# Performance work log

Measured on AMD Instinct MI355X. Metric: run time of the kernel, lower is better.

Reference implementation:

```python
import jax, jax.numpy as jnp
import numpy as np

NUM_ITERS = 20  # fixed in the original forward: transcribe(dna, iterations=20)


def transcribe(dna_seed, dna_a, dna_b):
    """Fractal DNA decompression: 20 elementwise contractive-map iterations
    over the full weight tensor, starting from the DNA seed."""
    def step(w, ab):
        a, b = ab
        w = a * w + b * jnp.sin(w)
        return w, None
    w, _ = jax.lax.scan(step, dna_seed, (dna_a, dna_b))
    return w  # [out_features, in_features]


def setup_inputs() -> dict:
    key = jax.random.key(0)
    k1, k2, k3, k4, k5 = jax.random.split(key, 5)
    TOKENS, IN_F, OUT_F = 2048, 4096, 4096
    return {
        "x": jax.random.normal(k1, (TOKENS, IN_F), dtype=jnp.float32),
        "dna_seed": jax.random.normal(k2, (OUT_F, IN_F), dtype=jnp.float32),
        "dna_a": jax.random.uniform(k3, (NUM_ITERS,), dtype=jnp.float32),
        "dna_b": jax.random.uniform(k4, (NUM_ITERS,), dtype=jnp.float32),
        "bias": jax.random.normal(k5, (OUT_F,), dtype=jnp.float32),
    }


def reference(x, dna_seed, dna_a, dna_b, bias):
    weight = transcribe(dna_seed, dna_a, dna_b)          # [out, in]
    # F.linear(x, weight, bias) == x @ weight.T + bias
    return jnp.einsum('ti,oi->to', x, weight) + bias     # [tokens, out]
```

## Files before the change

### kernel.cpp

```cpp
#include <hip/hip_runtime.h>

typedef __attribute__((ext_vector_type(8))) short short8;
typedef __attribute__((ext_vector_type(4))) float floatx4;
typedef __attribute__((ext_vector_type(2))) float float2v;

#define TOKENS 2048
#define IN_F   4096
#define OUT_F  4096
#define NITER  20

#define INV_2PI 0.15915494309189535f
#define TWO_PI  6.283185307179586f

__device__ __forceinline__ unsigned short f2bf(float f) {
    unsigned int u = __builtin_bit_cast(unsigned int, f);
    u += 0x7fffu + ((u >> 16) & 1u);
    return (unsigned short)(u >> 16);
}

__device__ __forceinline__ void step2(float2v& v, float2v a2, float2v bc2) {
    float2v s;
    s.x = __builtin_amdgcn_sinf(v.x);
    s.y = __builtin_amdgcn_sinf(v.y);
    v = __builtin_elementwise_fma(bc2, s, v * a2);
}

#define WBLOCKS (OUT_F * IN_F / 8 / 256)
#define XBLOCKS (TOKENS * IN_F / 8 / 256)

__global__ __launch_bounds__(256) void transcribe_fused_kernel(
    const float4* __restrict__ seed, const float4* __restrict__ xin,
    const float* __restrict__ da, const float* __restrict__ db,
    short8* __restrict__ w_out, short8* __restrict__ x_out)
{
    const int b = blockIdx.x;
    short8 o;
    if (b < WBLOCKS) {
        int i = b * 256 + threadIdx.x;
        float4 U = seed[2 * i];
        float4 V = seed[2 * i + 1];
        float2v p0 = {U.x, U.y}, p1 = {U.z, U.w};
        float2v p2 = {V.x, V.y}, p3 = {V.z, V.w};
        const float2v kinv = {INV_2PI, INV_2PI};
        p0 *= kinv; p1 *= kinv; p2 *= kinv; p3 *= kinv;
#pragma unroll
        for (int t = 0; t < NITER; t++) {
            float a = da[t], bc = db[t] * INV_2PI;
            float2v a2 = {a, a}, bc2 = {bc, bc};
            step2(p0, a2, bc2);
            step2(p1, a2, bc2);
            step2(p2, a2, bc2);
            step2(p3, a2, bc2);
        }
        o[0] = (short)f2bf(p0.x * TWO_PI); o[1] = (short)f2bf(p0.y * TWO_PI);
        o[2] = (short)f2bf(p1.x * TWO_PI); o[3] = (short)f2bf(p1.y * TWO_PI);
        o[4] = (short)f2bf(p2.x * TWO_PI); o[5] = (short)f2bf(p2.y * TWO_PI);
        o[6] = (short)f2bf(p3.x * TWO_PI); o[7] = (short)f2bf(p3.y * TWO_PI);
        w_out[i] = o;
    } else {
        int i = (b - WBLOCKS) * 256 + threadIdx.x;
        float4 u = xin[2 * i];
        float4 v = xin[2 * i + 1];
        o[0] = (short)f2bf(u.x); o[1] = (short)f2bf(u.y);
        o[2] = (short)f2bf(u.z); o[3] = (short)f2bf(u.w);
        o[4] = (short)f2bf(v.x); o[5] = (short)f2bf(v.y);
        o[6] = (short)f2bf(v.z); o[7] = (short)f2bf(v.w);
        x_out[i] = o;
    }
}

__device__ __forceinline__ void g2l16(const ushort* g, ushort* l) {
    __builtin_amdgcn_global_load_lds(
        (const __attribute__((address_space(1))) unsigned int*)g,
        (__attribute__((address_space(3))) unsigned int*)l, 16, 0, 0);
}

#define BK     64
#define BM     256
#define BN     128
#define NT     (IN_F / BK)
#define ASLOT  (BM * BK)
#define BSLOT  (BN * BK)
#define LDS_BYTES (3 * (ASLOT + BSLOT) * 2)

__global__ __launch_bounds__(512, 2) void gemm_bt_kernel(
    const ushort* __restrict__ A,
    const ushort* __restrict__ B,
    const float* __restrict__ bias,
    float* __restrict__ C)
{
    extern __shared__ ushort lds[];
    ushort* As = lds;
    ushort* Bs = lds + 3 * ASLOT;

    const int tid  = threadIdx.x;
    const int lane = tid & 63;
    const int wid  = tid >> 6;
    const int g    = wid >> 2;
    const int w2   = wid & 3;
    const int wm   = (w2 >> 1) << 7;
    const int wn   = (w2 & 1) << 6;
    const int fm   = lane & 15;
    const int q    = lane >> 4;

    const int bid = blockIdx.x;
    const int jj  = bid >> 3;
    const int bn  = (bid & 7) * 4 + (jj & 3);
    const int bm  = jj >> 2;

    const int gcol = (((lane & 7) ^ (lane >> 3)) << 3);

    const ushort* gA = A + (size_t)(bm * BM) * IN_F;
    const ushort* gB = B + (size_t)(bn * BN) * IN_F;

    floatx4 acc[8][4];
#pragma unroll
    for (int i = 0; i < 8; i++)
#pragma unroll
        for (int j = 0; j < 4; j++)
            acc[i][j] = (floatx4){0.f, 0.f, 0.f, 0.f};

#define STAGE(k0v, sl)                                                        \
    {                                                                         \
        _Pragma("unroll")                                                     \
        for (int u = 0; u < 4; u++) {                                         \
            const int cb = ((u << 3) | wid) << 6;                             \
            const int r  = (cb >> 3) + (lane >> 3);                           \
            g2l16(gA + (size_t)r * IN_F + (k0v) + gcol,                       \
                  As + (sl) * ASLOT + cb * 8 + lane * 8);                     \
        }                                                                     \
        _Pragma("unroll")                                                     \
        for (int u = 0; u < 2; u++) {                                         \
            const int cb = ((u << 3) | wid) << 6;                             \
            const int r  = (cb >> 3) + (lane >> 3);                           \
            g2l16(gB + (size_t)r * IN_F + (k0v) + gcol,                       \
                  Bs + (sl) * BSLOT + cb * 8 + lane * 8);                     \
        }                                                                     \
    }

#define LOADFRAG(sl)                                                          \
    const int sa = (((q + 4 * g) & 7) ^ (fm & 7)) << 3;                       \
    _Pragma("unroll")                                                         \
    for (int i = 0; i < 8; i++)                                               \
        af[i] = *(const short8*)(As + (sl) * ASLOT + (wm + i * 16 + fm) * BK + sa); \
    _Pragma("unroll")                                                         \
    for (int j = 0; j < 4; j++)                                               \
        bf[j] = *(const short8*)(Bs + (sl) * BSLOT + (wn + j * 16 + fm) * BK + sa);

#define MFMA32()                                                              \
    __builtin_amdgcn_s_setprio(1);                                            \
    _Pragma("unroll")                                                         \
    for (int i = 0; i < 8; i++)                                               \
        _Pragma("unroll")                                                     \
        for (int j = 0; j < 4; j++)                                           \
            acc[i][j] = __builtin_amdgcn_mfma_f32_16x16x32_bf16(              \
                af[i], bf[j], acc[i][j], 0, 0, 0);                            \
    __builtin_amdgcn_s_setprio(0);

#define TILE_MAIN(vm, sl, k3)                                                 \
    {                                                                         \
        asm volatile("s_waitcnt vmcnt(" #vm ")" ::: "memory");                \
        __builtin_amdgcn_s_barrier();                                         \
        short8 af[8], bf[4];                                                  \
        LOADFRAG(sl);                                                         \
        asm volatile("s_waitcnt lgkmcnt(0)" ::: "memory");                    \
        __builtin_amdgcn_s_barrier();                                         \
        STAGE(k3, sl);                                                        \
        __builtin_amdgcn_sched_barrier(0);                                    \
        MFMA32();                                                             \
    }

#define TILE_TAIL(vm, sl)                                                     \
    {                                                                         \
        asm volatile("s_waitcnt vmcnt(" #vm ")" ::: "memory");                \
        __builtin_amdgcn_s_barrier();                                         \
        short8 af[8], bf[4];                                                  \
        LOADFRAG(sl);                                                         \
        MFMA32();                                                             \
    }

    STAGE(0 * BK, 0);
    STAGE(1 * BK, 1);
    STAGE(2 * BK, 2);

    int st   = 0;
    int kpre = 3 * BK;
#pragma unroll 1
    for (int t = 0; t <= NT - 4; ++t) {
        TILE_MAIN(12, st, kpre);
        kpre += BK;
        st = (st == 2) ? 0 : st + 1;
    }
    TILE_TAIL(12, 1);
    TILE_TAIL(6, 2);
    TILE_TAIL(0, 0);

#undef STAGE
#undef LOADFRAG
#undef MFMA32
#undef TILE_MAIN
#undef TILE_TAIL

    __syncthreads();
    floatx4* red = (floatx4*)lds;
    if (g == 1) {
#pragma unroll
        for (int i = 0; i < 8; i++)
#pragma unroll
            for (int j = 0; j < 4; j++)
                red[(size_t)(w2 * 32 + i * 4 + j) * 64 + lane] = acc[i][j];
    }
    __syncthreads();
    if (g == 0) {
        const int cn = lane & 15;
        const int cm = (lane >> 4) << 2;
        float bv[4];
#pragma unroll
        for (int j = 0; j < 4; j++)
            bv[j] = bias[bn * BN + wn + j * 16 + cn];
#pragma unroll
        for (int i = 0; i < 8; i++) {
#pragma unroll
            for (int j = 0; j < 4; j++) {
                floatx4 p = red[(size_t)(w2 * 32 + i * 4 + j) * 64 + lane];
#pragma unroll
                for (int r = 0; r < 4; r++) acc[i][j][r] += p[r];
            }
#pragma unroll
            for (int r = 0; r < 4; r++) {
                int m = bm * BM + wm + i * 16 + cm + r;
                float* crow = C + (size_t)m * OUT_F + bn * BN + wn + cn;
#pragma unroll
                for (int j = 0; j < 4; j++)
                    crow[j * 16] = acc[i][j][r] + bv[j];
            }
        }
    }
}

extern "C" void kernel_launch(void* const* d_in, const int* in_sizes, int n_in,
                              void* d_out, int out_size, void* d_ws, size_t ws_size,
                              hipStream_t stream) {
    const float* x    = (const float*)d_in[0];
    const float* seed = (const float*)d_in[1];
    const float* da   = (const float*)d_in[2];
    const float* db   = (const float*)d_in[3];
    const float* bias = (const float*)d_in[4];
    float* out        = (float*)d_out;

    ushort* w_bf = (ushort*)d_ws;
    ushort* x_bf = w_bf + (size_t)OUT_F * IN_F;

    static bool lds_attr_set = false;
    if (!lds_attr_set) {
        hipFuncSetAttribute(reinterpret_cast<const void*>(gemm_bt_kernel),
                            hipFuncAttributeMaxDynamicSharedMemorySize,
                            LDS_BYTES);
        lds_attr_set = true;
    }

    transcribe_fused_kernel<<<WBLOCKS + XBLOCKS, 256, 0, stream>>>(
        (const float4*)seed, (const float4*)x, da, db,
        (short8*)w_bf, (short8*)x_bf);

    gemm_bt_kernel<<<dim3(32 * 8), dim3(512), LDS_BYTES, stream>>>(
        x_bf, w_bf, bias, out);
}
```

Baseline: 208.0 us.

## Split K in half and overlap second-half transcription with first-half GEMM

The transcription kernel now only produces the first half of the K dimension. A new mid kernel runs the first-half GEMM with 8 waves while 4 extra producer waves per block transcribe the second half of W and convert the second half of X to bf16. A final kernel accumulates the second-half GEMM into the output. This hides the sin-heavy transcription of half the weights behind MFMA work, but adds a read-modify-write of the output, one more launch, and a larger block (768 threads) that may reduce occupancy.

```diff
diff --git a/kernel.cpp b/kernel.cpp
--- a/kernel.cpp
+++ b/kernel.cpp
@@ -25,48 +25,86 @@
     v = __builtin_elementwise_fma(bc2, s, v * a2);
 }
 
-#define WBLOCKS (OUT_F * IN_F / 8 / 256)
-#define XBLOCKS (TOKENS * IN_F / 8 / 256)
-
-__global__ __launch_bounds__(256) void transcribe_fused_kernel(
-    const float4* __restrict__ seed, const float4* __restrict__ xin,
+
+#define T1_WBLK 4096
+#define T1_XBLK 2048
+
+__global__ __launch_bounds__(256) void transcribe_h1_kernel(
+    const float* __restrict__ seed, const float* __restrict__ xin,
     const float* __restrict__ da, const float* __restrict__ db,
-    short8* __restrict__ w_out, short8* __restrict__ x_out)
+    ushort* __restrict__ w_bf, ushort* __restrict__ x_bf)
 {
     const int b = blockIdx.x;
     short8 o;
-    if (b < WBLOCKS) {
-        int i = b * 256 + threadIdx.x;
-        float4 U = seed[2 * i];
-        float4 V = seed[2 * i + 1];
-        float2v p0 = {U.x, U.y}, p1 = {U.z, U.w};
-        float2v p2 = {V.x, V.y}, p3 = {V.z, V.w};
-        const float2v kinv = {INV_2PI, INV_2PI};
-        p0 *= kinv; p1 *= kinv; p2 *= kinv; p3 *= kinv;
+    if (b < T1_WBLK) {
+        const int i   = b * 256 + threadIdx.x;
+        const int row = i >> 8;
+        const int col = (i & 255) << 3;
+        const float* src = seed + (size_t)row * IN_F + col;
+        const float4 U = *(const float4*)src;
+        const float4 V = *(const float4*)(src + 4);
+        float2v p0 = {U.x * INV_2PI, U.y * INV_2PI};
+        float2v p1 = {U.z * INV_2PI, U.w * INV_2PI};
+        float2v p2 = {V.x * INV_2PI, V.y * INV_2PI};
+        float2v p3 = {V.z * INV_2PI, V.w * INV_2PI};
 #pragma unroll
         for (int t = 0; t < NITER; t++) {
-            float a = da[t], bc = db[t] * INV_2PI;
-            float2v a2 = {a, a}, bc2 = {bc, bc};
-            step2(p0, a2, bc2);
-            step2(p1, a2, bc2);
-            step2(p2, a2, bc2);
-            step2(p3, a2, bc2);
+            const float a = da[t], bc = db[t] * INV_2PI;
+            const float2v a2 = {a, a}, bc2 = {bc, bc};
+            step2(p0, a2, bc2); step2(p1, a2, bc2);
+            step2(p2, a2, bc2); step2(p3, a2, bc2);
         }
         o[0] = (short)f2bf(p0.x * TWO_PI); o[1] = (short)f2bf(p0.y * TWO_PI);
         o[2] = (short)f2bf(p1.x * TWO_PI); o[3] = (short)f2bf(p1.y * TWO_PI);
         o[4] = (short)f2bf(p2.x * TWO_PI); o[5] = (short)f2bf(p2.y * TWO_PI);
         o[6] = (short)f2bf(p3.x * TWO_PI); o[7] = (short)f2bf(p3.y * TWO_PI);
-        w_out[i] = o;
+        *(short8*)(w_bf + (size_t)row * IN_F + col) = o;
     } else {
-        int i = (b - WBLOCKS) * 256 + threadIdx.x;
-        float4 u = xin[2 * i];
-        float4 v = xin[2 * i + 1];
+        const int i   = (b - T1_WBLK) * 256 + threadIdx.x;
+        const int row = i >> 8;
+        const int col = (i & 255) << 3;
+        const float* src = xin + (size_t)row * IN_F + col;
+        const float4 u = *(const float4*)src;
+        const float4 v = *(const float4*)(src + 4);
         o[0] = (short)f2bf(u.x); o[1] = (short)f2bf(u.y);
         o[2] = (short)f2bf(u.z); o[3] = (short)f2bf(u.w);
         o[4] = (short)f2bf(v.x); o[5] = (short)f2bf(v.y);
         o[6] = (short)f2bf(v.z); o[7] = (short)f2bf(v.w);
-        x_out[i] = o;
-    }
+        *(short8*)(x_bf + (size_t)row * IN_F + col) = o;
+    }
+}
+
+__device__ __forceinline__ void produceW_f4(
+    int idx, const float* __restrict__ seed,
+    const float* __restrict__ da, const float* __restrict__ db,
+    ushort* __restrict__ w_bf)
+{
+    const int row = idx >> 9;
+    const int col = 2048 + ((idx & 511) << 2);
+    const float4 v = *(const float4*)(seed + (size_t)row * IN_F + col);
+    float2v p0 = {v.x * INV_2PI, v.y * INV_2PI};
+    float2v p1 = {v.z * INV_2PI, v.w * INV_2PI};
+#pragma unroll
+    for (int t = 0; t < NITER; t++) {
+        const float a = da[t], bc = db[t] * INV_2PI;
+        const float2v a2 = {a, a}, bc2 = {bc, bc};
+        step2(p0, a2, bc2); step2(p1, a2, bc2);
+    }
+    ushort4 o;
+    o.x = f2bf(p0.x * TWO_PI); o.y = f2bf(p0.y * TWO_PI);
+    o.z = f2bf(p1.x * TWO_PI); o.w = f2bf(p1.y * TWO_PI);
+    *(ushort4*)(w_bf + (size_t)row * IN_F + col) = o;
+}
+
+__device__ __forceinline__ void produceX_f4(
+    int idx, const float* __restrict__ xin, ushort* __restrict__ x_bf)
+{
+    const int row = idx >> 9;
+    const int col = 2048 + ((idx & 511) << 2);
+    const float4 v = *(const float4*)(xin + (size_t)row * IN_F + col);
+    ushort4 o;
+    o.x = f2bf(v.x); o.y = f2bf(v.y); o.z = f2bf(v.z); o.w = f2bf(v.w);
+    *(ushort4*)(x_bf + (size_t)row * IN_F + col) = o;
 }
 
 __device__ __forceinline__ void g2l16(const ushort* g, ushort* l) {
@@ -78,15 +116,182 @@
 #define BK     64
 #define BM     256
 #define BN     128
-#define NT     (IN_F / BK)
+#define NT2    32
 #define ASLOT  (BM * BK)
 #define BSLOT  (BN * BK)
 #define LDS_BYTES (3 * (ASLOT + BSLOT) * 2)
 
-__global__ __launch_bounds__(512, 2) void gemm_bt_kernel(
+#define STAGE(k0v, sl)                                                        \
+    {                                                                         \
+        _Pragma("unroll")                                                     \
+        for (int u = 0; u < 4; u++) {                                         \
+            const int cb = ((u << 3) | wid) << 6;                             \
+            const int r  = (cb >> 3) + (lane >> 3);                           \
+            g2l16(gA + (size_t)r * IN_F + (k0v) + gcol,                       \
+                  As + (sl) * ASLOT + cb * 8 + lane * 8);                     \
+        }                                                                     \
+        _Pragma("unroll")                                                     \
+        for (int u = 0; u < 2; u++) {                                         \
+            const int cb = ((u << 3) | wid) << 6;                             \
+            const int r  = (cb >> 3) + (lane >> 3);                           \
+            g2l16(gB + (size_t)r * IN_F + (k0v) + gcol,                       \
+                  Bs + (sl) * BSLOT + cb * 8 + lane * 8);                     \
+        }                                                                     \
+    }
+
+#define LOADFRAG(sl)                                                          \
+    const int sa = (((q + 4 * g) & 7) ^ (fm & 7)) << 3;                       \
+    _Pragma("unroll")                                                         \
+    for (int i = 0; i < 8; i++)                                               \
+        af[i] = *(const short8*)(As + (sl) * ASLOT + (wm + i * 16 + fm) * BK + sa); \
+    _Pragma("unroll")                                                         \
+    for (int j = 0; j < 4; j++)                                               \
+        bf[j] = *(const short8*)(Bs + (sl) * BSLOT + (wn + j * 16 + fm) * BK + sa);
+
+#define MFMA32()                                                              \
+    __builtin_amdgcn_s_setprio(1);                                            \
+    _Pragma("unroll")                                                         \
+    for (int i = 0; i < 8; i++)                                               \
+        _Pragma("unroll")                                                     \
+        for (int j = 0; j < 4; j++)                                           \
+            acc[i][j] = __builtin_amdgcn_mfma_f32_16x16x32_bf16(              \
+                af[i], bf[j], acc[i][j], 0, 0, 0);                            \
+    __builtin_amdgcn_s_setprio(0);
+
+#define GEMM_BODY()                                                           \
+    floatx4 acc[8][4];                                                        \
+    _Pragma("unroll")                                                         \
+    for (int i = 0; i < 8; i++)                                               \
+        _Pragma("unroll")                                                     \
+        for (int j = 0; j < 4; j++)                                           \
+            acc[i][j] = (floatx4){0.f, 0.f, 0.f, 0.f};                        \
+    STAGE(0 * BK, 0);                                                         \
+    STAGE(1 * BK, 1);                                                         \
+    STAGE(2 * BK, 2);                                                         \
+    int st   = 0;                                                             \
+    int kpre = 3 * BK;                                                        \
+    _Pragma("unroll 1")                                                       \
+    for (int t = 0; t <= NT2 - 4; ++t) {    \
+        asm volatile("s_waitcnt vmcnt(12)" ::: "memory");                     \
+        __builtin_amdgcn_s_barrier();                                         \
+        short8 af[8], bf[4];                                                  \
+        LOADFRAG(st);                                                         \
+        asm volatile("s_waitcnt lgkmcnt(0)" ::: "memory");                    \
+        __builtin_amdgcn_s_barrier();                                         \
+        STAGE(kpre, st);                                                      \
+        __builtin_amdgcn_sched_barrier(0);                                    \
+        MFMA32();                                                             \
+        kpre += BK;                                                           \
+        st = (st == 2) ? 0 : st + 1;                                          \
+    }                                                                         \
+                \
+    {                                                                         \
+        asm volatile("s_waitcnt vmcnt(12)" ::: "memory");                     \
+        __builtin_amdgcn_s_barrier();                                         \
+        short8 af[8], bf[4];                                                  \
+        LOADFRAG(2);                                                          \
+        MFMA32();                                                             \
+    }                                                                         \
+    {                                                                         \
+        asm volatile("s_waitcnt vmcnt(6)" ::: "memory");                      \
+        __builtin_amdgcn_s_barrier();                                         \
+        short8 af[8], bf[4];                                                  \
+        LOADFRAG(0);                                                          \
+        MFMA32();                                                             \
+    }                                                                         \
+    {                                                                         \
+        asm volatile("s_waitcnt vmcnt(0)" ::: "memory");                      \
+        __builtin_amdgcn_s_barrier();                                         \
+        short8 af[8], bf[4];                                                  \
+        LOADFRAG(1);                                                          \
+        MFMA32();                                                             \
+    }                                                                         \
+               \
+    __syncthreads();                                                          \
+    floatx4* red = (floatx4*)lds;                                             \
+    if (g == 1) {                                                             \
+        _Pragma("unroll")                                                     \
+        for (int i = 0; i < 8; i++)                                           \
+            _Pragma("unroll")                                                 \
+            for (int j = 0; j < 4; j++)                                       \
+                red[(size_t)(w2 * 32 + i * 4 + j) * 64 + lane] = acc[i][j];   \
+    }                                                                         \
+    __syncthreads();
+
+__global__ __launch_bounds__(768, 3) void fractal_mid_kernel(
+    const float* __restrict__ xin, const float* __restrict__ seed,
+    const float* __restrict__ da, const float* __restrict__ db,
+    const float* __restrict__ bias, float* __restrict__ C,
+    ushort* __restrict__ w_bf, ushort* __restrict__ x_bf)
+{
+    extern __shared__ ushort lds[];
+    ushort* As = lds;
+    ushort* Bs = lds + 3 * ASLOT;
+
+    const int tid  = threadIdx.x;
+    const int lane = tid & 63;
+    const int wid  = tid >> 6;
+    const int bid  = blockIdx.x;
+
+    if (wid >= 8) {
+        const int pid = (bid * 4 + (wid - 8)) * 64 + lane;
+#pragma unroll 1
+        for (int i = 0; i < 61; ++i) {
+            if (i < 32)      produceW_f4(pid + i * 65536, seed, da, db, w_bf);
+            else if (i < 48) produceX_f4(pid + (i - 32) * 65536, xin, x_bf);
+            __builtin_amdgcn_s_barrier();
+        }
+        __syncthreads();
+        __syncthreads();
+        return;
+    }
+
+    const int g    = wid >> 2;
+    const int w2   = wid & 3;
+    const int wm   = (w2 >> 1) << 7;
+    const int wn   = (w2 & 1) << 6;
+    const int fm   = lane & 15;
+    const int q    = lane >> 4;
+    const int jj   = bid >> 3;
+    const int bn   = (bid & 7) * 4 + (jj & 3);
+    const int bm   = jj >> 2;
+    const int gcol = (((lane & 7) ^ (lane >> 3)) << 3);
+
+    const ushort* gA = x_bf + (size_t)(bm * BM) * IN_F;
+    const ushort* gB = w_bf + (size_t)(bn * BN) * IN_F;
+
+    GEMM_BODY();
+
+    if (g == 0) {
+        const int cn = lane & 15;
+        const int cm = (lane >> 4) << 2;
+        float bv[4];
+#pragma unroll
+        for (int j = 0; j < 4; j++)
+            bv[j] = bias[bn * BN + wn + j * 16 + cn];
+#pragma unroll
+        for (int i = 0; i < 8; i++) {
+#pragma unroll
+            for (int j = 0; j < 4; j++) {
+                floatx4 p = red[(size_t)(w2 * 32 + i * 4 + j) * 64 + lane];
+#pragma unroll
+                for (int r = 0; r < 4; r++) acc[i][j][r] += p[r];
+            }
+#pragma unroll
+            for (int r = 0; r < 4; r++) {
+                int m = bm * BM + wm + i * 16 + cm + r;
+                float* crow = C + (size_t)m * OUT_F + bn * BN + wn + cn;
+#pragma unroll
+                for (int j = 0; j < 4; j++)
+                    crow[j * 16] = acc[i][j][r] + bv[j];
+            }
+        }
+    }
+}
+
+__global__ __launch_bounds__(512, 2) void gemm_k2_kernel(
     const ushort* __restrict__ A,
     const ushort* __restrict__ B,
-    const float* __restrict__ bias,
     float* __restrict__ C)
 {
     extern __shared__ ushort lds[];
@@ -102,141 +307,44 @@
     const int wn   = (w2 & 1) << 6;
     const int fm   = lane & 15;
     const int q    = lane >> 4;
-
-    const int bid = blockIdx.x;
-    const int jj  = bid >> 3;
-    const int bn  = (bid & 7) * 4 + (jj & 3);
-    const int bm  = jj >> 2;
-
+    const int bid  = blockIdx.x;
+    const int jj   = bid >> 3;
+    const int bn   = (bid & 7) * 4 + (jj & 3);
+    const int bm   = jj >> 2;
     const int gcol = (((lane & 7) ^ (lane >> 3)) << 3);
 
-    const ushort* gA = A + (size_t)(bm * BM) * IN_F;
-    const ushort* gB = B + (size_t)(bn * BN) * IN_F;
-
-    floatx4 acc[8][4];
-#pragma unroll
-    for (int i = 0; i < 8; i++)
-#pragma unroll
-        for (int j = 0; j < 4; j++)
-            acc[i][j] = (floatx4){0.f, 0.f, 0.f, 0.f};
-
-#define STAGE(k0v, sl)                                                        \
-    {                                                                         \
-        _Pragma("unroll")                                                     \
-        for (int u = 0; u < 4; u++) {                                         \
-            const int cb = ((u << 3) | wid) << 6;                             \
-            const int r  = (cb >> 3) + (lane >> 3);                           \
-            g2l16(gA + (size_t)r * IN_F + (k0v) + gcol,                       \
-                  As + (sl) * ASLOT + cb * 8 + lane * 8);                     \
-        }                                                                     \
-        _Pragma("unroll")                                                     \
-        for (int u = 0; u < 2; u++) {                                         \
-            const int cb = ((u << 3) | wid) << 6;                             \
-            const int r  = (cb >> 3) + (lane >> 3);                           \
-            g2l16(gB + (size_t)r * IN_F + (k0v) + gcol,                       \
-                  Bs + (sl) * BSLOT + cb * 8 + lane * 8);                     \
-        }                                                                     \
-    }
-
-#define LOADFRAG(sl)                                                          \
-    const int sa = (((q + 4 * g) & 7) ^ (fm & 7)) << 3;                       \
-    _Pragma("unroll")                                                         \
-    for (int i = 0; i < 8; i++)                                               \
-        af[i] = *(const short8*)(As + (sl) * ASLOT + (wm + i * 16 + fm) * BK + sa); \
-    _Pragma("unroll")                                                         \
-    for (int j = 0; j < 4; j++)                                               \
-        bf[j] = *(const short8*)(Bs + (sl) * BSLOT + (wn + j * 16 + fm) * BK + sa);
-
-#define MFMA32()                                                              \
-    __builtin_amdgcn_s_setprio(1);                                            \
-    _Pragma("unroll")                                                         \
-    for (int i = 0; i < 8; i++)                                               \
-        _Pragma("unroll")                                                     \
-        for (int j = 0; j < 4; j++)                                           \
-            acc[i][j] = __builtin_amdgcn_mfma_f32_16x16x32_bf16(              \
-                af[i], bf[j], acc[i][j], 0, 0, 0);                            \
-    __builtin_amdgcn_s_setprio(0);
-
-#define TILE_MAIN(vm, sl, k3)                                                 \
-    {                                                                         \
-        asm volatile("s_waitcnt vmcnt(" #vm ")" ::: "memory");                \
-        __builtin_amdgcn_s_barrier();                                         \
-        short8 af[8], bf[4];                                                  \
-        LOADFRAG(sl);                                                         \
-        asm volatile("s_waitcnt lgkmcnt(0)" ::: "memory");                    \
-        __builtin_amdgcn_s_barrier();                                         \
-        STAGE(k3, sl);                                                        \
-        __builtin_amdgcn_sched_barrier(0);                                    \
-        MFMA32();                                                             \
-    }
-
-#define TILE_TAIL(vm, sl)                                                     \
-    {                                                                         \
-        asm volatile("s_waitcnt vmcnt(" #vm ")" ::: "memory");                \
-        __builtin_amdgcn_s_barrier();                                         \
-        short8 af[8], bf[4];                                                  \
-        LOADFRAG(sl);                                                         \
-        MFMA32();                                                             \
-    }
-
-    STAGE(0 * BK, 0);
-    STAGE(1 * BK, 1);
-    STAGE(2 * BK, 2);
-
-    int st   = 0;
-    int kpre = 3 * BK;
-#pragma unroll 1
-    for (int t = 0; t <= NT - 4; ++t) {
-        TILE_MAIN(12, st, kpre);
-        kpre += BK;
-        st = (st == 2) ? 0 : st + 1;
-    }
-    TILE_TAIL(12, 1);
-    TILE_TAIL(6, 2);
-    TILE_TAIL(0, 0);
+    const ushort* gA = A + (size_t)(bm * BM) * IN_F + 2048;
+    const ushort* gB = B + (size_t)(bn * BN) * IN_F + 2048;
+
+    GEMM_BODY();
+
+    if (g == 0) {
+        const int cn = lane & 15;
+        const int cm = (lane >> 4) << 2;
+#pragma unroll
+        for (int i = 0; i < 8; i++) {
+#pragma unroll
+            for (int j = 0; j < 4; j++) {
+                floatx4 p = red[(size_t)(w2 * 32 + i * 4 + j) * 64 + lane];
+#pragma unroll
+                for (int r = 0; r < 4; r++) acc[i][j][r] += p[r];
+            }
+#pragma unroll
+            for (int r = 0; r < 4; r++) {
+                int m = bm * BM + wm + i * 16 + cm + r;
+                float* crow = C + (size_t)m * OUT_F + bn * BN + wn + cn;
+#pragma unroll
+                for (int j = 0; j < 4; j++)
+                    crow[j * 16] += acc[i][j][r];
+            }
+        }
+    }
+}
 
 #undef STAGE
 #undef LOADFRAG
 #undef MFMA32
-#undef TILE_MAIN
-#undef TILE_TAIL
-
-    __syncthreads();
-    floatx4* red = (floatx4*)lds;
-    if (g == 1) {
-#pragma unroll
-        for (int i = 0; i < 8; i++)
-#pragma unroll
-            for (int j = 0; j < 4; j++)
-                red[(size_t)(w2 * 32 + i * 4 + j) * 64 + lane] = acc[i][j];
-    }
-    __syncthreads();
-    if (g == 0) {
-        const int cn = lane & 15;
-        const int cm = (lane >> 4) << 2;
-        float bv[4];
-#pragma unroll
-        for (int j = 0; j < 4; j++)
-            bv[j] = bias[bn * BN + wn + j * 16 + cn];
-#pragma unroll
-        for (int i = 0; i < 8; i++) {
-#pragma unroll
-            for (int j = 0; j < 4; j++) {
-                floatx4 p = red[(size_t)(w2 * 32 + i * 4 + j) * 64 + lane];
-#pragma unroll
-                for (int r = 0; r < 4; r++) acc[i][j][r] += p[r];
-            }
-#pragma unroll
-            for (int r = 0; r < 4; r++) {
-                int m = bm * BM + wm + i * 16 + cm + r;
-                float* crow = C + (size_t)m * OUT_F + bn * BN + wn + cn;
-#pragma unroll
-                for (int j = 0; j < 4; j++)
-                    crow[j * 16] = acc[i][j][r] + bv[j];
-            }
-        }
-    }
-}
+#undef GEMM_BODY
 
 extern "C" void kernel_launch(void* const* d_in, const int* in_sizes, int n_in,
                               void* d_out, int out_size, void* d_ws, size_t ws_size,
@@ -253,16 +361,19 @@
 
     static bool lds_attr_set = false;
     if (!lds_attr_set) {
-        hipFuncSetAttribute(reinterpret_cast<const void*>(gemm_bt_kernel),
+        hipFuncSetAttribute(reinterpret_cast<const void*>(fractal_mid_kernel),
+                            hipFuncAttributeMaxDynamicSharedMemorySize,
+                            LDS_BYTES);
+        hipFuncSetAttribute(reinterpret_cast<const void*>(gemm_k2_kernel),
                             hipFuncAttributeMaxDynamicSharedMemorySize,
                             LDS_BYTES);
         lds_attr_set = true;
     }
 
-    transcribe_fused_kernel<<<WBLOCKS + XBLOCKS, 256, 0, stream>>>(
-        (const float4*)seed, (const float4*)x, da, db,
-        (short8*)w_bf, (short8*)x_bf);
-
-    gemm_bt_kernel<<<dim3(32 * 8), dim3(512), LDS_BYTES, stream>>>(
-        x_bf, w_bf, bias, out);
-}
+    transcribe_h1_kernel<<<T1_WBLK + T1_XBLK, 256, 0, stream>>>(
+        seed, x, da, db, w_bf, x_bf);
+    fractal_mid_kernel<<<dim3(256), dim3(768), LDS_BYTES, stream>>>(
+        x, seed, da, db, bias, out, w_bf, x_bf);
+    gemm_k2_kernel<<<dim3(256), dim3(512), LDS_BYTES, stream>>>(
+        x_bf, w_bf, out);
+}
```

Result: slower. 370.9 us (+78.4%).
